# Kernel tuning notes

Measured on AMD Instinct MI355X. Metric: run time of the kernel, lower is better.

The kernel has to match this reference:

```python
import jax, jax.numpy as jnp
import numpy as np

IN_FEATURES = 512
OUT_FEATURES = 512
BATCH = 1024


def setup_inputs() -> dict:
    key = jax.random.key(0)
    k_x, k_bw, k_ww, k_sc, k_tr, k_b = jax.random.split(key, 6)
    std = 1.0 / np.sqrt(IN_FEATURES)
    x = jax.random.normal(k_x, (BATCH, IN_FEATURES), dtype=jnp.float32)
    base_weight = jax.random.uniform(k_bw, (OUT_FEATURES, IN_FEATURES), jnp.float32, -std, std)
    wavelet_weights = jax.random.uniform(k_ww, (OUT_FEATURES, IN_FEATURES), jnp.float32, -std, std)
    # scale initialized to ones in the module; perturb slightly (kept positive) for a non-degenerate test
    scale = jnp.exp(0.1 * jax.random.normal(k_sc, (OUT_FEATURES, IN_FEATURES), dtype=jnp.float32))
    translation = 0.1 * jax.random.normal(k_tr, (OUT_FEATURES, IN_FEATURES), dtype=jnp.float32)
    bias = jax.random.uniform(k_b, (OUT_FEATURES,), jnp.float32, -std, std)
    return {"x": x, "base_weight": base_weight, "wavelet_weights": wavelet_weights,
            "scale": scale, "translation": translation, "bias": bias}


def reference(x, base_weight, wavelet_weights, scale, translation, bias):
    # base branch: SiLU then linear
    base_out = jnp.einsum("bi,oi->bo", jax.nn.silu(x), base_weight)
    # wavelet branch: broadcast x to (batch, out, in)
    xs = (x[:, None, :] - translation[None, :, :]) / scale[None, :, :]  # (B, O, I)
    wavelet = (xs * xs - 1.0) * jnp.exp(-0.5 * xs * xs)  # mexican hat
    wavelet_out = jnp.einsum("boi,oi->bo", wavelet, wavelet_weights)
    return base_out + wavelet_out + bias
```

## Files before the change

kernel.cpp:

```cpp
#include <hip/hip_runtime.h>


constexpr int IN_F  = 512;
constexpr int OUT_F = 512;
constexpr int BATCH = 1024;
constexpr int BT = 64, OT = 64;
constexpr int IT = 16;
constexpr int PITCH = IT + 4;
constexpr int HP = IT + 4;
constexpr int LP = OT + 1;
constexpr int BO  = BATCH * OUT_F;

#define LOG2E 1.44269504088897f
#define C2f   (-0.72134752044448f)
#define NC2f  ( 0.72134752044448f)
#define RQf   (-0.84083003f)

typedef float v2f   __attribute__((ext_vector_type(2)));
typedef float f32x4 __attribute__((ext_vector_type(4)));
typedef _Float16 half4 __attribute__((ext_vector_type(4)));

__device__ __forceinline__ float fexp2(float v) { return __builtin_amdgcn_exp2f(v); }
__device__ __forceinline__ float frcp(float v)  { return __builtin_amdgcn_rcpf(v); }
__device__ __forceinline__ v2f pkfma(v2f a, v2f b, v2f c) {
  return __builtin_elementwise_fma(a, b, c);
}
__device__ __forceinline__ float fsilu(float v) {
  return v * frcp(1.f + fexp2(v * -LOG2E));
}

constexpr int SMEM_F = 7680;

template<int KS>
__global__ __launch_bounds__(256, 2)
void wkan_main(const float* __restrict__ x, const float* __restrict__ basew,
               const float* __restrict__ wavew, const float* __restrict__ scale,
               const float* __restrict__ transl, const float* __restrict__ bias,
               float* __restrict__ partial, float* __restrict__ out, int use_ws)
{
  constexpr int KR  = IN_F / KS;
  constexpr int NCH = KR / IT;

  __shared__ float smem[SMEM_F];
  float* lx = smem;
  float* la = smem + 1280;
  float* lm = smem + 2560;
  float* ln = smem + 3840;
  float* lq = smem + 5120;
  _Float16* hx = (_Float16*)(smem + 6400);
  _Float16* hb = (_Float16*)(smem + 7040);
  float* lout = smem;

  const int tid = threadIdx.x;
  const int b0 = blockIdx.x * BT;
  const int o0 = blockIdx.y * OT;
  const int ks = blockIdx.z;
  const int k0 = ks * KR;

  const int srow = tid >> 2;
  const int sc4  = (tid & 3) * 4;
  const int lofs = srow * PITCH + sc4;
  const int hofs = srow * HP + sc4;

  const int to = tid & 15;
  const int tb = tid >> 4;

  const int lane = tid & 63;
  const int wid  = tid >> 6;
  const int frow = lane & 15;
  const int kgrp = (lane >> 4) * 4;

  v2f zz; zz.x = 0.f; zz.y = 0.f;
  v2f acc[4][4];
#pragma unroll
  for (int r = 0; r < 4; ++r)
#pragma unroll
    for (int c = 0; c < 4; ++c) acc[r][c] = zz;

  f32x4 accb[4];
#pragma unroll
  for (int nt = 0; nt < 4; ++nt) accb[nt] = (f32x4)0.f;

  for (int kc = 0; kc < NCH; ++kc) {
    const int g = k0 + kc * IT + sc4;
    if (kc) __syncthreads();
    {
      float4 xv = *(const float4*)(x + (size_t)(b0 + srow) * IN_F + g);
      float4 sx;
      sx.x = fsilu(xv.x); sx.y = fsilu(xv.y); sx.z = fsilu(xv.z); sx.w = fsilu(xv.w);
      *(float4*)(lx + lofs) = xv;
      half4 h0;
      h0[0] = (_Float16)sx.x; h0[1] = (_Float16)sx.y;
      h0[2] = (_Float16)sx.z; h0[3] = (_Float16)sx.w;
      *(half4*)(hx + hofs) = h0;

      float4 sv = *(const float4*)(scale  + (size_t)(o0 + srow) * IN_F + g);
      float4 tv = *(const float4*)(transl + (size_t)(o0 + srow) * IN_F + g);
      float4 av, mv, nv;
      {
        float a2, a2t;
        a2 = C2f * frcp(sv.x * sv.x); a2t = a2 * tv.x;
        av.x = a2; mv.x = -2.f * a2t; nv.x = fmaf(a2t, tv.x, NC2f);
        a2 = C2f * frcp(sv.y * sv.y); a2t = a2 * tv.y;
        av.y = a2; mv.y = -2.f * a2t; nv.y = fmaf(a2t, tv.y, NC2f);
        a2 = C2f * frcp(sv.z * sv.z); a2t = a2 * tv.z;
        av.z = a2; mv.z = -2.f * a2t; nv.z = fmaf(a2t, tv.z, NC2f);
        a2 = C2f * frcp(sv.w * sv.w); a2t = a2 * tv.w;
        av.w = a2; mv.w = -2.f * a2t; nv.w = fmaf(a2t, tv.w, NC2f);
      }
      *(float4*)(la + lofs) = av;
      *(float4*)(lm + lofs) = mv;
      *(float4*)(ln + lofs) = nv;

      float4 wv = *(const float4*)(wavew + (size_t)(o0 + srow) * IN_F + g);
      float4 qv;
      qv.x = wv.x * RQf; qv.y = wv.y * RQf; qv.z = wv.z * RQf; qv.w = wv.w * RQf;
      *(float4*)(lq + lofs) = qv;

      float4 bv = *(const float4*)(basew + (size_t)(o0 + srow) * IN_F + g);
      half4 hbv;
      hbv[0] = (_Float16)bv.x; hbv[1] = (_Float16)bv.y;
      hbv[2] = (_Float16)bv.z; hbv[3] = (_Float16)bv.w;
      *(half4*)(hb + hofs) = hbv;
    }
    __syncthreads();

    {
      half4 af = *(const half4*)(hx + (wid * 16 + frow) * HP + kgrp);
#pragma unroll
      for (int nt = 0; nt < 4; ++nt) {
        half4 bf = *(const half4*)(hb + (nt * 16 + frow) * HP + kgrp);
        accb[nt] = __builtin_amdgcn_mfma_f32_16x16x16f16(af, bf, accb[nt], 0, 0, 0);
      }
    }

    for (int ii = 0; ii < IT; ii += 4) {
      float4 xr[4];
#pragma unroll
      for (int r = 0; r < 4; ++r) {
        const int row = (tb + 16 * r) * PITCH + ii;
        xr[r] = *(const float4*)(lx + row);
      }
#pragma unroll
      for (int c = 0; c < 4; ++c) {
        const int orow = (to + 16 * c) * PITCH + ii;
        float4 A = *(const float4*)(la + orow);
        float4 M = *(const float4*)(lm + orow);
        float4 N = *(const float4*)(ln + orow);
        float4 Q = *(const float4*)(lq + orow);
        v2f Al = {A.x, A.y}, Ah = {A.z, A.w};
        v2f Ml = {M.x, M.y}, Mh = {M.z, M.w};
        v2f Nl = {N.x, N.y}, Nh = {N.z, N.w};
        v2f Ql = {Q.x, Q.y}, Qh = {Q.z, Q.w};
#pragma unroll
        for (int r = 0; r < 4; ++r) {
          v2f xl  = {xr[r].x, xr[r].y}, xh  = {xr[r].z, xr[r].w};
          v2f p, e, gg;
          p = pkfma(pkfma(Al, xl, Ml), xl, Nl);
          e.x = fexp2(p.x); e.y = fexp2(p.y);
          gg = p * Ql;
          acc[r][c] = pkfma(gg, e, acc[r][c]);
          p = pkfma(pkfma(Ah, xh, Mh), xh, Nh);
          e.x = fexp2(p.x); e.y = fexp2(p.y);
          gg = p * Qh;
          acc[r][c] = pkfma(gg, e, acc[r][c]);
        }
      }
    }
  }

  __syncthreads();
#pragma unroll
  for (int nt = 0; nt < 4; ++nt)
#pragma unroll
    for (int i = 0; i < 4; ++i)
      lout[(wid * 16 + (lane >> 4) * 4 + i) * LP + nt * 16 + frow] = accb[nt][i];
  __syncthreads();

#pragma unroll
  for (int r = 0; r < 4; ++r) {
    const int br = b0 + tb + 16 * r;
#pragma unroll
    for (int c = 0; c < 4; ++c) {
      const int oc = o0 + to + 16 * c;
      float res = acc[r][c].x + acc[r][c].y
                + lout[(tb + 16 * r) * LP + to + 16 * c];
      if (use_ws) {
        partial[(size_t)ks * BO + (size_t)br * OUT_F + oc] = res;
      } else {
        if (ks == 0) res += bias[oc];
        atomicAdd(out + (size_t)br * OUT_F + oc, res);
      }
    }
  }
}

template<int KS>
__global__ __launch_bounds__(256)
void wkan_reduce(const float* __restrict__ partial, const float* __restrict__ bias,
                 float* __restrict__ out)
{
  const int i4 = (blockIdx.x * 256 + threadIdx.x) * 4;
  float4 r = *(const float4*)(bias + (i4 & (OUT_F - 1)));
#pragma unroll
  for (int k = 0; k < KS; ++k) {
    float4 a = *(const float4*)(partial + (size_t)k * BO + i4);
    r.x += a.x; r.y += a.y; r.z += a.z; r.w += a.w;
  }
  *(float4*)(out + i4) = r;
}

extern "C" void kernel_launch(void* const* d_in, const int* in_sizes, int n_in,
                              void* d_out, int out_size, void* d_ws, size_t ws_size,
                              hipStream_t stream) {
  const float* x  = (const float*)d_in[0];
  const float* bw = (const float*)d_in[1];
  const float* ww = (const float*)d_in[2];
  const float* sc = (const float*)d_in[3];
  const float* tr = (const float*)d_in[4];
  const float* bi = (const float*)d_in[5];
  float* out = (float*)d_out;

  if (ws_size >= (size_t)16 * BO * sizeof(float)) {
    dim3 grid(BATCH / BT, OUT_F / OT, 16);
    wkan_main<16><<<grid, dim3(256), 0, stream>>>(x, bw, ww, sc, tr, bi,
                                                  (float*)d_ws, out, 1);
    wkan_reduce<16><<<dim3(BO / 1024), dim3(256), 0, stream>>>((const float*)d_ws, bi, out);
  } else if (ws_size >= (size_t)8 * BO * sizeof(float)) {
    dim3 grid(BATCH / BT, OUT_F / OT, 8);
    wkan_main<8><<<grid, dim3(256), 0, stream>>>(x, bw, ww, sc, tr, bi,
                                                 (float*)d_ws, out, 1);
    wkan_reduce<8><<<dim3(BO / 1024), dim3(256), 0, stream>>>((const float*)d_ws, bi, out);
  } else {
    hipMemsetAsync(d_out, 0, (size_t)out_size * sizeof(float), stream);
    dim3 grid(BATCH / BT, OUT_F / OT, 8);
    wkan_main<8><<<grid, dim3(256), 0, stream>>>(x, bw, ww, sc, tr, bi,
                                                 (float*)d_ws, out, 0);
  }
}
```

Baseline: 110.3 us.

## Double batch tile to 128 rows per block for more operand reuse

Raises the batch tile from 64 to 128 rows. Each thread now computes 8x4 wavelet outputs instead of 4x4, and each wave issues two MFMA row tiles for the base branch. This reuses the per-output scale, translation and weight coefficients loaded from shared memory across twice as many batch rows, which cuts LDS traffic per exp evaluation and halves the grid. The costs are higher register pressure (64 accumulators plus 8 x float4 vectors), more shared memory, and half as many blocks, which may reduce occupancy.

Measured after the change: 113.6 us. 1.03x slower.

```diff
diff --git a/kernel.cpp b/kernel.cpp
--- a/kernel.cpp
+++ b/kernel.cpp
@@ -4,7 +4,7 @@
 constexpr int IN_F  = 512;
 constexpr int OUT_F = 512;
 constexpr int BATCH = 1024;
-constexpr int BT = 64, OT = 64;
+constexpr int BT = 128, OT = 64;
 constexpr int IT = 16;
 constexpr int PITCH = IT + 4;
 constexpr int HP = IT + 4;
@@ -29,7 +29,7 @@
   return v * frcp(1.f + fexp2(v * -LOG2E));
 }
 
-constexpr int SMEM_F = 7680;
+constexpr int SMEM_F = 9600;
 
 template<int KS>
 __global__ __launch_bounds__(256, 2)
@@ -43,12 +43,12 @@
 
   __shared__ float smem[SMEM_F];
   float* lx = smem;
-  float* la = smem + 1280;
-  float* lm = smem + 2560;
-  float* ln = smem + 3840;
-  float* lq = smem + 5120;
-  _Float16* hx = (_Float16*)(smem + 6400);
-  _Float16* hb = (_Float16*)(smem + 7040);
+  float* la = smem + 2560;
+  float* lm = smem + 3840;
+  float* ln = smem + 5120;
+  float* lq = smem + 6400;
+  _Float16* hx = (_Float16*)(smem + 7680);
+  _Float16* hb = (_Float16*)(smem + 8960);
   float* lout = smem;
 
   const int tid = threadIdx.x;
@@ -71,28 +71,36 @@
   const int kgrp = (lane >> 4) * 4;
 
   v2f zz; zz.x = 0.f; zz.y = 0.f;
-  v2f acc[4][4];
-#pragma unroll
-  for (int r = 0; r < 4; ++r)
+  v2f acc[8][4];
+#pragma unroll
+  for (int r = 0; r < 8; ++r)
 #pragma unroll
     for (int c = 0; c < 4; ++c) acc[r][c] = zz;
 
-  f32x4 accb[4];
-#pragma unroll
-  for (int nt = 0; nt < 4; ++nt) accb[nt] = (f32x4)0.f;
+  f32x4 accb[2][4];
+#pragma unroll
+  for (int mt = 0; mt < 2; ++mt)
+#pragma unroll
+    for (int nt = 0; nt < 4; ++nt) accb[mt][nt] = (f32x4)0.f;
 
   for (int kc = 0; kc < NCH; ++kc) {
     const int g = k0 + kc * IT + sc4;
     if (kc) __syncthreads();
     {
-      float4 xv = *(const float4*)(x + (size_t)(b0 + srow) * IN_F + g);
-      float4 sx;
-      sx.x = fsilu(xv.x); sx.y = fsilu(xv.y); sx.z = fsilu(xv.z); sx.w = fsilu(xv.w);
-      *(float4*)(lx + lofs) = xv;
-      half4 h0;
-      h0[0] = (_Float16)sx.x; h0[1] = (_Float16)sx.y;
-      h0[2] = (_Float16)sx.z; h0[3] = (_Float16)sx.w;
+      float4 xv0 = *(const float4*)(x + (size_t)(b0 + srow)      * IN_F + g);
+      float4 xv1 = *(const float4*)(x + (size_t)(b0 + srow + 64) * IN_F + g);
+      float4 sx0, sx1;
+      sx0.x = fsilu(xv0.x); sx0.y = fsilu(xv0.y); sx0.z = fsilu(xv0.z); sx0.w = fsilu(xv0.w);
+      sx1.x = fsilu(xv1.x); sx1.y = fsilu(xv1.y); sx1.z = fsilu(xv1.z); sx1.w = fsilu(xv1.w);
+      *(float4*)(lx + lofs) = xv0;
+      *(float4*)(lx + lofs + 64 * PITCH) = xv1;
+      half4 h0, h1;
+      h0[0] = (_Float16)sx0.x; h0[1] = (_Float16)sx0.y;
+      h0[2] = (_Float16)sx0.z; h0[3] = (_Float16)sx0.w;
+      h1[0] = (_Float16)sx1.x; h1[1] = (_Float16)sx1.y;
+      h1[2] = (_Float16)sx1.z; h1[3] = (_Float16)sx1.w;
       *(half4*)(hx + hofs) = h0;
+      *(half4*)(hx + hofs + 64 * HP) = h1;
 
       float4 sv = *(const float4*)(scale  + (size_t)(o0 + srow) * IN_F + g);
       float4 tv = *(const float4*)(transl + (size_t)(o0 + srow) * IN_F + g);
@@ -126,18 +134,20 @@
     __syncthreads();
 
     {
-      half4 af = *(const half4*)(hx + (wid * 16 + frow) * HP + kgrp);
+      half4 af0 = *(const half4*)(hx + (wid * 32 +      frow) * HP + kgrp);
+      half4 af1 = *(const half4*)(hx + (wid * 32 + 16 + frow) * HP + kgrp);
 #pragma unroll
       for (int nt = 0; nt < 4; ++nt) {
         half4 bf = *(const half4*)(hb + (nt * 16 + frow) * HP + kgrp);
-        accb[nt] = __builtin_amdgcn_mfma_f32_16x16x16f16(af, bf, accb[nt], 0, 0, 0);
+        accb[0][nt] = __builtin_amdgcn_mfma_f32_16x16x16f16(af0, bf, accb[0][nt], 0, 0, 0);
+        accb[1][nt] = __builtin_amdgcn_mfma_f32_16x16x16f16(af1, bf, accb[1][nt], 0, 0, 0);
       }
     }
 
     for (int ii = 0; ii < IT; ii += 4) {
-      float4 xr[4];
-#pragma unroll
-      for (int r = 0; r < 4; ++r) {
+      float4 xr[8];
+#pragma unroll
+      for (int r = 0; r < 8; ++r) {
         const int row = (tb + 16 * r) * PITCH + ii;
         xr[r] = *(const float4*)(lx + row);
       }
@@ -153,7 +163,7 @@
         v2f Nl = {N.x, N.y}, Nh = {N.z, N.w};
         v2f Ql = {Q.x, Q.y}, Qh = {Q.z, Q.w};
 #pragma unroll
-        for (int r = 0; r < 4; ++r) {
+        for (int r = 0; r < 8; ++r) {
           v2f xl  = {xr[r].x, xr[r].y}, xh  = {xr[r].z, xr[r].w};
           v2f p, e, gg;
           p = pkfma(pkfma(Al, xl, Ml), xl, Nl);
@@ -171,14 +181,17 @@
 
   __syncthreads();
 #pragma unroll
-  for (int nt = 0; nt < 4; ++nt)
-#pragma unroll
-    for (int i = 0; i < 4; ++i)
-      lout[(wid * 16 + (lane >> 4) * 4 + i) * LP + nt * 16 + frow] = accb[nt][i];
+  for (int mt = 0; mt < 2; ++mt)
+#pragma unroll
+    for (int nt = 0; nt < 4; ++nt)
+#pragma unroll
+      for (int i = 0; i < 4; ++i)
+        lout[(wid * 32 + mt * 16 + (lane >> 4) * 4 + i) * LP + nt * 16 + frow]
+            = accb[mt][nt][i];
   __syncthreads();
 
 #pragma unroll
-  for (int r = 0; r < 4; ++r) {
+  for (int r = 0; r < 8; ++r) {
     const int br = b0 + tb + 16 * r;
 #pragma unroll
     for (int c = 0; c < 4; ++c) {
```
